# Performance work log

Measured on AMD Instinct MI355X. Metric: run time of the kernel, lower is better.

Reference implementation:

```python
import jax, jax.numpy as jnp
import numpy as np

B, LQ, LK, E, H = 8, 1024, 1024, 512, 8
D = E // H
NEG = -2.0**32 + 1  # padding value used by original torch code


def setup_inputs() -> dict:
    key = jax.random.key(0)
    ks = jax.random.split(key, 6)
    s = 0.02
    return {
        "x1": jax.random.normal(ks[0], (B, LQ, E), jnp.float32),
        "x2": jax.random.normal(ks[1], (B, LK, E), jnp.float32),
        "Wq": jax.random.normal(ks[2], (E, E), jnp.float32) * s,
        "bq": jnp.zeros((E,), jnp.float32),
        "Wk": jax.random.normal(ks[3], (E, E), jnp.float32) * s,
        "bk": jnp.zeros((E,), jnp.float32),
        "Wv": jax.random.normal(ks[4], (E, E), jnp.float32) * s,
        "bv": jnp.zeros((E,), jnp.float32),
    }


def _split_heads(t):
    # torch: cat(split(t, E//H, dim=2), dim=0) -> head-major [H, B, L, D]
    b, l, _ = t.shape
    return jnp.moveaxis(t.reshape(b, l, H, D), 2, 0)


def reference(x1, x2, Wq, bq, Wk, bk, Wv, bv):
    # ReLU-activated projections (nn.Linear: x @ W.T + b)
    q = jax.nn.relu(x1 @ Wq.T + bq)  # [B,LQ,E]
    k = jax.nn.relu(x2 @ Wk.T + bk)  # [B,LK,E]
    v = jax.nn.relu(x2 @ Wv.T + bv)  # [B,LK,E]

    q_, k_, v_ = _split_heads(q), _split_heads(k), _split_heads(v)  # [H,B,L,D]

    # scaled scores; original scales by sqrt(emb_size), not sqrt(d_head)
    scores = jnp.einsum('hbqd,hbkd->hbqk', q_, k_) / jnp.sqrt(jnp.float32(E))

    # sin-based key mask from raw x2
    key_mask = jnp.sin(jnp.abs(jnp.sum(x2, -1)))  # [B,LK]
    scores = jnp.where(key_mask[None, :, None, :] <= 0, NEG, scores)

    attn = jax.nn.softmax(scores, axis=-1)

    # sin-based query mask from raw x1, applied after softmax
    query_mask = jnp.sin(jnp.abs(jnp.sum(x1, -1)))  # [B,LQ]
    attn = attn * query_mask[None, :, :, None]

    out = jnp.einsum('hbqk,hbkd->hbqd', attn, v_)  # [H,B,LQ,D]
    out = jnp.moveaxis(out, 0, 2).reshape(B, LQ, E)  # merge heads back
    return out + q  # residual add with activated query projection
```

## Files before the change

### kernel.cpp

```cpp
#include <hip/hip_runtime.h>
#include <hip/hip_bf16.h>
#include <math.h>

typedef short bf16x8 __attribute__((ext_vector_type(8)));
typedef float f32x4 __attribute__((ext_vector_type(4)));
typedef unsigned int u32;
typedef unsigned short u16;

constexpr int Bb = 8, LQn = 1024, LKn = 1024, En = 512, Hn = 8, Dn = 64;
constexpr int Mtok = Bb * LQn;
constexpr float KCOEF = 0.06376246332977306f;

__device__ __forceinline__ u16 f2bf(float f) {
  u32 u = __builtin_bit_cast(u32, f);
  u32 r = (u + 0x7fffu + ((u >> 16) & 1u)) >> 16;
  return (u16)r;
}
__device__ __forceinline__ float bf2f(u16 h) {
  u32 u = ((u32)h) << 16;
  return __builtin_bit_cast(float, u);
}
__device__ __forceinline__ u16 f2bf_hw(float f) {
  return __builtin_bit_cast(u16, __float2bfloat16(f));
}

__device__ __forceinline__ void async_lds16(const void* gsrc, void* ldst) {
  __builtin_amdgcn_global_load_lds(
      (const __attribute__((address_space(1))) u32*)gsrc,
      (__attribute__((address_space(3))) u32*)ldst, 16, 0, 0);
}

__global__ void prep_kernel(const float* __restrict__ x1, const float* __restrict__ x2,
                            u16* __restrict__ x1b, u16* __restrict__ x2b,
                            float* __restrict__ qmask, float* __restrict__ kmask,
                            const float* __restrict__ Wq, const float* __restrict__ Wk,
                            const float* __restrict__ Wv, u16* __restrict__ wqb,
                            u16* __restrict__ wkb, u16* __restrict__ wvb) {
  int blk = blockIdx.x;
  if (blk < 4096) {
    int id = blk * 4 + (threadIdx.x >> 6);
    int lane = threadIdx.x & 63;
    const float* x; u16* xb; float* mask; int row;
    if (id < Mtok) { x = x1; xb = x1b; mask = qmask; row = id; }
    else           { x = x2; xb = x2b; mask = kmask; row = id - Mtok; }
    const float4* p = reinterpret_cast<const float4*>(x + (size_t)row * En);
    ushort4* ob = reinterpret_cast<ushort4*>(xb + (size_t)row * En);
    double s = 0.0;
#pragma unroll
    for (int j = 0; j < En / 256; ++j) {
      float4 v = p[lane + j * 64];
      s += (double)v.x + (double)v.y + (double)v.z + (double)v.w;
      ushort4 o;
      o.x = f2bf(v.x); o.y = f2bf(v.y); o.z = f2bf(v.z); o.w = f2bf(v.w);
      ob[lane + j * 64] = o;
    }
#pragma unroll
    for (int off = 32; off > 0; off >>= 1) s += __shfl_down(s, off, 64);
    if (lane == 0) mask[row] = (float)sin(fabs(s));
  } else {
    int n4 = En * En / 4;
    int j = (blk - 4096) * 256 + threadIdx.x;
    const float* src; u16* dst;
    if (j < n4) { src = Wq; dst = wqb; }
    else if (j < 2 * n4) { src = Wk; dst = wkb; j -= n4; }
    else { src = Wv; dst = wvb; j -= 2 * n4; }
    float4 v = reinterpret_cast<const float4*>(src)[j];
    ushort4 o;
    o.x = f2bf(v.x); o.y = f2bf(v.y); o.z = f2bf(v.z); o.w = f2bf(v.w);
    reinterpret_cast<ushort4*>(dst)[j] = o;
  }
}

template <int BIAS_ROW>
__device__ __forceinline__ void gemm_core(
    const u16* __restrict__ A, const u16* __restrict__ Bm,
    const float* __restrict__ bias, u16* __restrict__ C,
    int ldc, float coef, int row0, int col0) {
  constexpr int K = 512, BK = 64;
  __shared__ u16 sA[2][128 * BK];
  __shared__ u16 sB[2][128 * BK];
  int tid = threadIdx.x;
  int lane = tid & 63;
  int w = tid >> 6;
  int wm = w >> 2, wn = w & 3;
  int rgrp = lane >> 4, cidx = lane & 15;

  f32x4 acc[4][2];
#pragma unroll
  for (int mi = 0; mi < 4; ++mi)
#pragma unroll
    for (int ni = 0; ni < 2; ++ni) acc[mi][ni] = f32x4{0.f, 0.f, 0.f, 0.f};

  auto stage = [&](int kt, int buf) {
    int k0 = kt * BK;
#pragma unroll
    for (int rr = 0; rr < 2; ++rr) {
      int cid = rr * 512 + tid;
      int r = cid >> 3, c = cid & 7;
      int cg = c ^ (r & 7);
      async_lds16(A + (size_t)(row0 + r) * K + k0 + cg * 8, &sA[buf][cid * 8]);
    }
#pragma unroll
    for (int rr = 0; rr < 2; ++rr) {
      int cid = rr * 512 + tid;
      int r = cid >> 3, c = cid & 7;
      int cg = c ^ (r & 7);
      async_lds16(Bm + (size_t)(col0 + r) * K + k0 + cg * 8, &sB[buf][cid * 8]);
    }
  };

  stage(0, 0);
  __syncthreads();

  for (int kt = 0; kt < K / BK; ++kt) {
    int cur = kt & 1;
    if (kt < K / BK - 1) stage(kt + 1, cur ^ 1);
#pragma unroll
    for (int kk = 0; kk < 2; ++kk) {
      bf16x8 a[4], b[2];
#pragma unroll
      for (int mi = 0; mi < 4; ++mi) {
        int row = wm * 64 + mi * 16 + cidx;
        a[mi] = *reinterpret_cast<const bf16x8*>(
            &sA[cur][row * BK + ((kk * 4 + rgrp) ^ (row & 7)) * 8]);
      }
#pragma unroll
      for (int ni = 0; ni < 2; ++ni) {
        int row = wn * 32 + ni * 16 + cidx;
        b[ni] = *reinterpret_cast<const bf16x8*>(
            &sB[cur][row * BK + ((kk * 4 + rgrp) ^ (row & 7)) * 8]);
      }
#pragma unroll
      for (int mi = 0; mi < 4; ++mi)
#pragma unroll
        for (int ni = 0; ni < 2; ++ni)
          acc[mi][ni] = __builtin_amdgcn_mfma_f32_16x16x32_bf16(a[mi], b[ni], acc[mi][ni], 0, 0, 0);
    }
    __syncthreads();
  }
#pragma unroll
  for (int mi = 0; mi < 4; ++mi)
#pragma unroll
    for (int ni = 0; ni < 2; ++ni)
#pragma unroll
      for (int r = 0; r < 4; ++r) {
        int grow = row0 + wm * 64 + mi * 16 + rgrp * 4 + r;
        int gcol = col0 + wn * 32 + ni * 16 + cidx;
        float v = acc[mi][ni][r] + (BIAS_ROW ? bias[grow] : bias[gcol]);
        v = v > 0.f ? v : 0.f;
        C[(size_t)grow * ldc + gcol] = f2bf(v * coef);
      }
}

__global__ __launch_bounds__(512, 4) void gemm3(
    const u16* __restrict__ x1b, const u16* __restrict__ wqb, const float* __restrict__ bq,
    u16* __restrict__ qbq,
    const u16* __restrict__ x2b, const u16* __restrict__ wkb, const float* __restrict__ bk,
    u16* __restrict__ kbk,
    const u16* __restrict__ wvb, const float* __restrict__ bv, u16* __restrict__ vtb) {
  int z = blockIdx.z;
  if (z == 0) {
    gemm_core<0>(x1b, wqb, bq, qbq, En, 1.0f, blockIdx.x * 128, blockIdx.y * 128);
  } else if (z == 1) {
    gemm_core<0>(x2b, wkb, bk, kbk, En, KCOEF, blockIdx.x * 128, blockIdx.y * 128);
  } else {
    gemm_core<1>(wvb, x2b, bv, vtb, Mtok, 1.0f, blockIdx.y * 128, blockIdx.x * 128);
  }
}

__global__ __launch_bounds__(256, 4) void attn_kernel(
    const u16* __restrict__ qb, const u16* __restrict__ kb, const u16* __restrict__ vtb,
    const float* __restrict__ kmask, const float* __restrict__ qmask,
    float* __restrict__ out) {
  __shared__ u16 sK[2][64 * 64];
  __shared__ u16 sV[2][64 * 64];
  __shared__ u16 sQP[64 * 64];
  int tid = threadIdx.x, lane = tid & 63, w = tid >> 6;
  int bh = blockIdx.x, qblk = blockIdx.y;
  int b = bh >> 3, h = bh & 7;
  int rgrp = lane >> 4, cidx = lane & 15;

  const u16* qbase = qb + ((size_t)(b * LQn) + qblk * 64) * En + h * Dn;
  const u16* kbase = kb + (size_t)(b * LKn) * En + h * Dn;
  const u16* vbase = vtb + (size_t)(h * Dn) * Mtok + b * LKn;
  const float* kmb = kmask + b * LKn;

  auto stageKV = [&](int kt, int buf) {
#pragma unroll
    for (int rr = 0; rr < 2; ++rr) {
      int cid = rr * 256 + tid;
      int r = cid >> 3, c = cid & 7;
      int cg = c ^ (r & 7);
      async_lds16(kbase + (size_t)(kt * 64 + r) * En + cg * 8, &sK[buf][cid * 8]);
      async_lds16(vbase + (size_t)r * Mtok + kt * 64 + cg * 8, &sV[buf][cid * 8]);
    }
  };

#pragma unroll
  for (int rr = 0; rr < 2; ++rr) {
    int cid = rr * 256 + tid;
    int r = cid >> 3, c = cid & 7;
    int cg = c ^ (r & 7);
    async_lds16(qbase + (size_t)r * En + cg * 8, &sQP[cid * 8]);
  }
  stageKV(0, 0);
  __syncthreads();

  bf16x8 qa[2];
  {
    int row = w * 16 + cidx;
    qa[0] = *reinterpret_cast<const bf16x8*>(&sQP[row * 64 + (rgrp ^ (row & 7)) * 8]);
    qa[1] = *reinterpret_cast<const bf16x8*>(&sQP[row * 64 + ((4 + rgrp) ^ (row & 7)) * 8]);
  }

  f32x4 acc_o[4];
#pragma unroll
  for (int dt = 0; dt < 4; ++dt) acc_o[dt] = f32x4{0.f, 0.f, 0.f, 0.f};
  float den = 0.f;

  int prow = w * 16 + cidx;
  char* sPbyte = reinterpret_cast<char*>(sQP);

  for (int kt = 0; kt < LKn / 64; ++kt) {
    int cur = kt & 1;
    if (kt < LKn / 64 - 1) stageKV(kt + 1, cur ^ 1);
#pragma unroll
    for (int ktile = 0; ktile < 4; ++ktile) {
      int krow = ktile * 16 + cidx;
      bf16x8 kf0 = *reinterpret_cast<const bf16x8*>(
          &sK[cur][krow * 64 + (rgrp ^ (krow & 7)) * 8]);
      bf16x8 kf1 = *reinterpret_cast<const bf16x8*>(
          &sK[cur][krow * 64 + ((4 + rgrp) ^ (krow & 7)) * 8]);
      float4 km4 = *reinterpret_cast<const float4*>(&kmb[kt * 64 + ktile * 16 + rgrp * 4]);
      f32x4 s;
      s[0] = km4.x > 0.f ? 0.f : -3.0e38f;
      s[1] = km4.y > 0.f ? 0.f : -3.0e38f;
      s[2] = km4.z > 0.f ? 0.f : -3.0e38f;
      s[3] = km4.w > 0.f ? 0.f : -3.0e38f;
      s = __builtin_amdgcn_mfma_f32_16x16x32_bf16(kf0, qa[0], s, 0, 0, 0);
      s = __builtin_amdgcn_mfma_f32_16x16x32_bf16(kf1, qa[1], s, 0, 0, 0);
      float p0 = __builtin_amdgcn_exp2f(s[0]);
      float p1 = __builtin_amdgcn_exp2f(s[1]);
      float p2 = __builtin_amdgcn_exp2f(s[2]);
      float p3 = __builtin_amdgcn_exp2f(s[3]);
      den += (p0 + p1) + (p2 + p3);
      ushort4 pk;
      pk.x = f2bf_hw(p0); pk.y = f2bf_hw(p1); pk.z = f2bf_hw(p2); pk.w = f2bf_hw(p3);
      int gran = ktile * 2 + (rgrp >> 1);
      int boff = prow * 128 + ((gran ^ (prow & 7)) << 4) + ((rgrp & 1) << 3);
      *reinterpret_cast<ushort4*>(sPbyte + boff) = pk;
    }
    __builtin_amdgcn_s_setprio(1);
#pragma unroll
    for (int kk = 0; kk < 2; ++kk) {
      bf16x8 pa = *reinterpret_cast<const bf16x8*>(
          &sQP[prow * 64 + ((kk * 4 + rgrp) ^ (prow & 7)) * 8]);
#pragma unroll
      for (int dt = 0; dt < 4; ++dt) {
        int vrow = dt * 16 + cidx;
        bf16x8 vf = *reinterpret_cast<const bf16x8*>(
            &sV[cur][vrow * 64 + ((kk * 4 + rgrp) ^ (vrow & 7)) * 8]);
        acc_o[dt] = __builtin_amdgcn_mfma_f32_16x16x32_bf16(pa, vf, acc_o[dt], 0, 0, 0);
      }
    }
    __builtin_amdgcn_s_setprio(0);
    __syncthreads();
  }
  den += __shfl_xor(den, 16, 64);
  den += __shfl_xor(den, 32, 64);

  const float* qmb = qmask + (size_t)b * LQn + qblk * 64 + w * 16;
  const u16* qres = qbase + (size_t)(w * 16) * En;
  float* obase = out + ((size_t)(b * LQn) + qblk * 64 + w * 16) * En + h * Dn;
#pragma unroll
  for (int r = 0; r < 4; ++r) {
    int qr = rgrp * 4 + r;
    float denq = __shfl(den, qr, 64);
    float fac = qmb[qr] / denq;
#pragma unroll
    for (int dt = 0; dt < 4; ++dt) {
      float v = acc_o[dt][r] * fac + bf2f(qres[(size_t)qr * En + dt * 16 + cidx]);
      obase[(size_t)qr * En + dt * 16 + cidx] = v;
    }
  }
}

extern "C" void kernel_launch(void* const* d_in, const int* in_sizes, int n_in,
                              void* d_out, int out_size, void* d_ws, size_t ws_size,
                              hipStream_t stream) {
  const float* x1 = (const float*)d_in[0];
  const float* x2 = (const float*)d_in[1];
  const float* Wq = (const float*)d_in[2];
  const float* bq = (const float*)d_in[3];
  const float* Wk = (const float*)d_in[4];
  const float* bk = (const float*)d_in[5];
  const float* Wv = (const float*)d_in[6];
  const float* bv = (const float*)d_in[7];
  float* out = (float*)d_out;

  char* ws = (char*)d_ws;
  size_t o = 0;
  u16* x1b = (u16*)(ws + o); o += (size_t)Mtok * En * 2;
  u16* x2b = (u16*)(ws + o); o += (size_t)Mtok * En * 2;
  u16* wqb = (u16*)(ws + o); o += (size_t)En * En * 2;
  u16* wkb = (u16*)(ws + o); o += (size_t)En * En * 2;
  u16* wvb = (u16*)(ws + o); o += (size_t)En * En * 2;
  u16* qbq = (u16*)(ws + o); o += (size_t)Mtok * En * 2;
  u16* kbk = (u16*)(ws + o); o += (size_t)Mtok * En * 2;
  u16* vtb = (u16*)(ws + o); o += (size_t)Mtok * En * 2;
  float* kmask = (float*)(ws + o); o += (size_t)Mtok * 4;
  float* qmask = (float*)(ws + o); o += (size_t)Mtok * 4;

  prep_kernel<<<4864, 256, 0, stream>>>(x1, x2, x1b, x2b, qmask, kmask,
                                        Wq, Wk, Wv, wqb, wkb, wvb);

  dim3 g3(Mtok / 128, En / 128, 3);
  gemm3<<<g3, 512, 0, stream>>>(x1b, wqb, bq, qbq, x2b, wkb, bk, kbk, wvb, bv, vtb);

  dim3 ga(Bb * Hn, LQn / 64);
  attn_kernel<<<ga, 256, 0, stream>>>(qbq, kbk, vtb, kmask, qmask, out);
}
```

Measured before the change: 71.43 us.

## Load K and V fragments directly from global memory instead of LDS staging

Removes the double-buffered async LDS staging of K and V tiles (and Q) in the attention kernel. Each wave now reads its MFMA fragments straight from global memory, relying on L1/L2 reuse across the four waves, and only keeps a small LDS buffer for P. Dropping per-iteration block barriers and the LDS footprint allows a higher occupancy hint (6 blocks per CU). The trade-off is redundant global/L1 traffic (each wave reloads the same K/V fragments) and exposed load latency without explicit prefetch.

```diff
diff --git a/kernel.cpp b/kernel.cpp
--- a/kernel.cpp
+++ b/kernel.cpp
@@ -168,13 +168,11 @@
   }
 }
 
-__global__ __launch_bounds__(256, 4) void attn_kernel(
+__global__ __launch_bounds__(256, 6) void attn_kernel(
     const u16* __restrict__ qb, const u16* __restrict__ kb, const u16* __restrict__ vtb,
     const float* __restrict__ kmask, const float* __restrict__ qmask,
     float* __restrict__ out) {
-  __shared__ u16 sK[2][64 * 64];
-  __shared__ u16 sV[2][64 * 64];
-  __shared__ u16 sQP[64 * 64];
+  __shared__ u16 sP[64 * 64];
   int tid = threadIdx.x, lane = tid & 63, w = tid >> 6;
   int bh = blockIdx.x, qblk = blockIdx.y;
   int b = bh >> 3, h = bh & 7;
@@ -185,33 +183,9 @@
   const u16* vbase = vtb + (size_t)(h * Dn) * Mtok + b * LKn;
   const float* kmb = kmask + b * LKn;
 
-  auto stageKV = [&](int kt, int buf) {
-#pragma unroll
-    for (int rr = 0; rr < 2; ++rr) {
-      int cid = rr * 256 + tid;
-      int r = cid >> 3, c = cid & 7;
-      int cg = c ^ (r & 7);
-      async_lds16(kbase + (size_t)(kt * 64 + r) * En + cg * 8, &sK[buf][cid * 8]);
-      async_lds16(vbase + (size_t)r * Mtok + kt * 64 + cg * 8, &sV[buf][cid * 8]);
-    }
-  };
-
-#pragma unroll
-  for (int rr = 0; rr < 2; ++rr) {
-    int cid = rr * 256 + tid;
-    int r = cid >> 3, c = cid & 7;
-    int cg = c ^ (r & 7);
-    async_lds16(qbase + (size_t)r * En + cg * 8, &sQP[cid * 8]);
-  }
-  stageKV(0, 0);
-  __syncthreads();
-
-  bf16x8 qa[2];
-  {
-    int row = w * 16 + cidx;
-    qa[0] = *reinterpret_cast<const bf16x8*>(&sQP[row * 64 + (rgrp ^ (row & 7)) * 8]);
-    qa[1] = *reinterpret_cast<const bf16x8*>(&sQP[row * 64 + ((4 + rgrp) ^ (row & 7)) * 8]);
-  }
+  int qrow = w * 16 + cidx;
+  bf16x8 qa0 = *reinterpret_cast<const bf16x8*>(qbase + (size_t)qrow * En + rgrp * 8);
+  bf16x8 qa1 = *reinterpret_cast<const bf16x8*>(qbase + (size_t)qrow * En + 32 + rgrp * 8);
 
   f32x4 acc_o[4];
 #pragma unroll
@@ -219,26 +193,23 @@
   float den = 0.f;
 
   int prow = w * 16 + cidx;
-  char* sPbyte = reinterpret_cast<char*>(sQP);
+  char* sPbyte = reinterpret_cast<char*>(sP);
 
   for (int kt = 0; kt < LKn / 64; ++kt) {
-    int cur = kt & 1;
-    if (kt < LKn / 64 - 1) stageKV(kt + 1, cur ^ 1);
 #pragma unroll
     for (int ktile = 0; ktile < 4; ++ktile) {
-      int krow = ktile * 16 + cidx;
-      bf16x8 kf0 = *reinterpret_cast<const bf16x8*>(
-          &sK[cur][krow * 64 + (rgrp ^ (krow & 7)) * 8]);
-      bf16x8 kf1 = *reinterpret_cast<const bf16x8*>(
-          &sK[cur][krow * 64 + ((4 + rgrp) ^ (krow & 7)) * 8]);
+      int krow = kt * 64 + ktile * 16 + cidx;
+      const u16* kp = kbase + (size_t)krow * En + rgrp * 8;
+      bf16x8 kf0 = *reinterpret_cast<const bf16x8*>(kp);
+      bf16x8 kf1 = *reinterpret_cast<const bf16x8*>(kp + 32);
       float4 km4 = *reinterpret_cast<const float4*>(&kmb[kt * 64 + ktile * 16 + rgrp * 4]);
       f32x4 s;
       s[0] = km4.x > 0.f ? 0.f : -3.0e38f;
       s[1] = km4.y > 0.f ? 0.f : -3.0e38f;
       s[2] = km4.z > 0.f ? 0.f : -3.0e38f;
       s[3] = km4.w > 0.f ? 0.f : -3.0e38f;
-      s = __builtin_amdgcn_mfma_f32_16x16x32_bf16(kf0, qa[0], s, 0, 0, 0);
-      s = __builtin_amdgcn_mfma_f32_16x16x32_bf16(kf1, qa[1], s, 0, 0, 0);
+      s = __builtin_amdgcn_mfma_f32_16x16x32_bf16(kf0, qa0, s, 0, 0, 0);
+      s = __builtin_amdgcn_mfma_f32_16x16x32_bf16(kf1, qa1, s, 0, 0, 0);
       float p0 = __builtin_amdgcn_exp2f(s[0]);
       float p1 = __builtin_amdgcn_exp2f(s[1]);
       float p2 = __builtin_amdgcn_exp2f(s[2]);
@@ -254,17 +225,15 @@
 #pragma unroll
     for (int kk = 0; kk < 2; ++kk) {
       bf16x8 pa = *reinterpret_cast<const bf16x8*>(
-          &sQP[prow * 64 + ((kk * 4 + rgrp) ^ (prow & 7)) * 8]);
+          &sP[prow * 64 + ((kk * 4 + rgrp) ^ (prow & 7)) * 8]);
 #pragma unroll
       for (int dt = 0; dt < 4; ++dt) {
-        int vrow = dt * 16 + cidx;
-        bf16x8 vf = *reinterpret_cast<const bf16x8*>(
-            &sV[cur][vrow * 64 + ((kk * 4 + rgrp) ^ (vrow & 7)) * 8]);
+        const u16* vp = vbase + (size_t)(dt * 16 + cidx) * Mtok + kt * 64 + kk * 32 + rgrp * 8;
+        bf16x8 vf = *reinterpret_cast<const bf16x8*>(vp);
         acc_o[dt] = __builtin_amdgcn_mfma_f32_16x16x32_bf16(pa, vf, acc_o[dt], 0, 0, 0);
       }
     }
     __builtin_amdgcn_s_setprio(0);
-    __syncthreads();
   }
   den += __shfl_xor(den, 16, 64);
   den += __shfl_xor(den, 32, 64);
```

Measured after the change: 163.5 us. 2.29x slower.
